# Kernel tuning notes

Measured on AMD Instinct MI355X. Metric: run time of the kernel, lower is better.

## Reference

```python
import jax, jax.numpy as jnp
import numpy as np

HIDDEN = 512
HEADS = 8
HEAD_DIM = HIDDEN // HEADS


def setup_inputs() -> dict:
    key = jax.random.key(0)
    ks = jax.random.split(key, 12)
    B, N, C = 4, 2048, HIDDEN
    s = 1.0 / np.sqrt(C)
    inp = {
        "query_content": jax.random.normal(ks[0], (B, N, C), dtype=jnp.float32),
        "query_pos": jax.random.uniform(ks[1], (B, N, 4), dtype=jnp.float32),
        "Wq": jax.random.uniform(ks[2], (C, C), jnp.float32, -s, s),
        "bq": jax.random.uniform(ks[3], (C,), jnp.float32, -s, s),
        "Wk": jax.random.uniform(ks[4], (C, C), jnp.float32, -s, s),
        "bk": jax.random.uniform(ks[5], (C,), jnp.float32, -s, s),
        "Wv": jax.random.uniform(ks[6], (C, C), jnp.float32, -s, s),
        "bv": jax.random.uniform(ks[7], (C,), jnp.float32, -s, s),
        "Wo": jax.random.uniform(ks[8], (C, C), jnp.float32, -s, s),
        "bo": jax.random.uniform(ks[9], (C,), jnp.float32, -s, s),
        "gamma": jnp.ones((C,), jnp.float32),
        "beta": jnp.zeros((C,), jnp.float32),
    }
    return inp


def _iof_bias(query_pos):
    # query_pos: [B, N, 4] -> bias [B, N, N] = -0.1 * sqrt(dx^2 + dy^2 + eps)
    x = query_pos[..., 0]
    y = query_pos[..., 1]
    dx = jnp.abs(x[:, :, None] - x[:, None, :])
    dy = jnp.abs(y[:, :, None] - y[:, None, :])
    dist = jnp.sqrt(dx * dx + dy * dy + 1e-8)
    return -0.1 * dist


def reference(query_content, query_pos, Wq, bq, Wk, bk, Wv, bv, Wo, bo, gamma, beta):
    B, N, C = query_content.shape
    H, D = HEADS, HEAD_DIM
    # torch Linear: x @ W.T + b
    Q = (query_content @ Wq.T + bq).reshape(B, N, H, D).transpose(0, 2, 1, 3)
    K = (query_content @ Wk.T + bk).reshape(B, N, H, D).transpose(0, 2, 1, 3)
    V = (query_content @ Wv.T + bv).reshape(B, N, H, D).transpose(0, 2, 1, 3)
    scores = jnp.einsum("bhnd,bhmd->bhnm", Q, K) / jnp.sqrt(jnp.float32(D))
    scores = scores + _iof_bias(query_pos)[:, None, :, :]
    attn = jax.nn.softmax(scores, axis=-1)
    out = jnp.einsum("bhnm,bhmd->bhnd", attn, V)
    out = out.transpose(0, 2, 1, 3).reshape(B, N, C)
    out = out @ Wo.T + bo
    h = out + query_content
    mu = jnp.mean(h, axis=-1, keepdims=True)
    var = jnp.var(h, axis=-1, keepdims=True)
    return (h - mu) / jnp.sqrt(var + 1e-5) * gamma + beta
```

## Files before the change

### kernel.cpp

```cpp
#include <hip/hip_runtime.h>
#include <hip/hip_bf16.h>

#define C_DIM 512
#define H_NUM 8
#define D_DIM 64
#define B_NUM 4
#define N_SEQ 2048
#define M_TOT (B_NUM*N_SEQ)

typedef unsigned short u16;
typedef unsigned int   u32;
typedef __attribute__((ext_vector_type(8))) short short8;
typedef __attribute__((ext_vector_type(4))) float f32x4;

#define MFMA16 __builtin_amdgcn_mfma_f32_16x16x32_bf16

__device__ __forceinline__ u16 f2b(float f) {
    union { float f; u32 u; } v; v.f = f;
    u32 r = v.u + 0x7FFFu + ((v.u >> 16) & 1u);
    return (u16)(r >> 16);
}
__device__ __forceinline__ float fexp2(float x) {
    float r;
    asm("v_exp_f32 %0, %1" : "=v"(r) : "v"(x));
    return r;
}
__device__ __forceinline__ float b2f_lo(u32 u) {
    union { u32 u; float f; } v; v.u = u << 16; return v.f;
}
__device__ __forceinline__ float b2f_hi(u32 u) {
    union { u32 u; float f; } v; v.u = u & 0xFFFF0000u; return v.f;
}
__device__ __forceinline__ void gload16(const u16* g, u16* l) {
    __builtin_amdgcn_global_load_lds(
        (const __attribute__((address_space(1))) void*)g,
        (__attribute__((address_space(3))) void*)l, 16, 0, 0);
}
__device__ __forceinline__ void cast8(const float* s, u16* d) {
    const float4* p = (const float4*)s;
    float4 a = p[0], b = p[1];
    short8 v;
    v[0] = (short)f2b(a.x); v[1] = (short)f2b(a.y);
    v[2] = (short)f2b(a.z); v[3] = (short)f2b(a.w);
    v[4] = (short)f2b(b.x); v[5] = (short)f2b(b.y);
    v[6] = (short)f2b(b.z); v[7] = (short)f2b(b.w);
    *(short8*)d = v;
}

__global__ __launch_bounds__(256) void k_prep(const float* __restrict__ qc,
                                              const float* __restrict__ Wq,
                                              const float* __restrict__ Wk,
                                              const float* __restrict__ Wv,
                                              const float* __restrict__ Wo,
                                              const float* __restrict__ bq,
                                              const float* __restrict__ bk,
                                              const float* __restrict__ bv,
                                              const float* __restrict__ bo,
                                              const float* __restrict__ qpos,
                                              u16* __restrict__ xb,
                                              u16* __restrict__ wb,
                                              float* __restrict__ bqkv,
                                              u16* __restrict__ bias)
{
    const int bid = blockIdx.x, t = threadIdx.x;
    if (bid < 2048) {
        int i = bid * 256 + t;
        cast8(qc + (size_t)i * 8, xb + (size_t)i * 8);
    } else if (bid < 2560) {
        int r = bid - 2048;
        int y = r >> 7;
        const float* s = (y == 0) ? Wq : (y == 1) ? Wk : (y == 2) ? Wv : Wo;
        int i = (r & 127) * 256 + t;
        cast8(s + (size_t)i * 8, wb + (size_t)y * 262144 + (size_t)i * 8);
    } else if (bid < 2568) {
        int idx = (bid - 2560) * 256 + t;
        float v = idx < 512 ? bq[idx] : idx < 1024 ? bk[idx - 512]
                : idx < 1536 ? bv[idx - 1024] : bo[idx - 1536];
        bqkv[idx] = v;
    } else {
        int r = bid - 2568;
        int i = r & 2047, b = r >> 11;
        const float4 qi = *(const float4*)(qpos + (size_t)(b * 2048 + i) * 4);
        const float4* pj = (const float4*)(qpos + ((size_t)b * 2048 + t * 8) * 4);
        const float NC = -0.1f * 1.4426950408889634f;
        short8 v;
        #pragma unroll
        for (int jj = 0; jj < 8; ++jj) {
            float4 pk = pj[jj];
            float dx = qi.x - pk.x, dy = qi.y - pk.y;
            float d2 = fmaf(dx, dx, fmaf(dy, dy, 1e-8f));
            v[jj] = (short)f2b(sqrtf(d2) * NC);
        }
        *(short8*)(bias + (size_t)(b * 2048 + i) * 2048 + t * 8) = v;
    }
}

__global__ __launch_bounds__(256) void k_gemm(const u16* __restrict__ A,
                                              const u16* __restrict__ Bw,
                                              const float* __restrict__ bias,
                                              const float* __restrict__ qc,
                                              u16* __restrict__ oq,
                                              u16* __restrict__ ok,
                                              u16* __restrict__ ov,
                                              float* __restrict__ outf,
                                              int fixed_mode)
{
    __shared__ alignas(16) u16 smem[24576];
    typedef u16 (*Tbuf)[4][128][8];
    Tbuf la = (Tbuf)smem;
    Tbuf lb = (Tbuf)(smem + 12288);
    const int t = threadIdx.x;
    const int nwg = gridDim.x * gridDim.y;
    const int wgid = blockIdx.y * gridDim.x + blockIdx.x;
    const int swz = (wgid & 7) * (nwg >> 3) + (wgid >> 3);
    const int ntn = gridDim.y;
    const int m0 = (swz / ntn) * 128, n0 = (swz % ntn) * 128;
    const int w = t >> 6, l = t & 63, lr = l & 15, kg = l >> 4;
    const int wm = w >> 1, wn = w & 1;
    const int NS = C_DIM / 32;

    f32x4 acc[4][4] = {};

    const int srow = t & 127;
    const u16* As0 = A + (size_t)(m0 + srow) * C_DIM + (t >> 7) * 8;
    const u16* Bs0 = Bw + (size_t)(n0 + srow) * C_DIM + (t >> 7) * 8;

    #pragma unroll
    for (int s = 0; s < 2; ++s) {
        u16* ldA = (u16*)la[s] + w * 512;
        u16* ldB = (u16*)lb[s] + w * 512;
        gload16(As0 + s * 32,      ldA);
        gload16(As0 + s * 32 + 16, ldA + 2048);
        gload16(Bs0 + s * 32,      ldB);
        gload16(Bs0 + s * 32 + 16, ldB + 2048);
    }
    asm volatile("s_waitcnt vmcnt(4)" ::: "memory");
    __builtin_amdgcn_s_barrier();

    for (int s = 0; s < NS; ++s) {
        const int bi = s % 3;
        if (s + 2 < NS) {
            const int bn = (s + 2) % 3;
            u16* ldA = (u16*)la[bn] + w * 512;
            u16* ldB = (u16*)lb[bn] + w * 512;
            gload16(As0 + (s + 2) * 32,      ldA);
            gload16(As0 + (s + 2) * 32 + 16, ldA + 2048);
            gload16(Bs0 + (s + 2) * 32,      ldB);
            gload16(Bs0 + (s + 2) * 32 + 16, ldB + 2048);
        }
        __builtin_amdgcn_sched_barrier(0);

        short8 af[4], bf[4];
        #pragma unroll
        for (int fm = 0; fm < 4; ++fm)
            af[fm] = *(const short8*)la[bi][kg][wm * 64 + fm * 16 + lr];
        #pragma unroll
        for (int fn = 0; fn < 4; ++fn)
            bf[fn] = *(const short8*)lb[bi][kg][wn * 64 + fn * 16 + lr];
        __builtin_amdgcn_s_setprio(1);
        #pragma unroll
        for (int fm = 0; fm < 4; ++fm)
        #pragma unroll
        for (int fn = 0; fn < 4; ++fn)
            acc[fm][fn] = MFMA16(af[fm], bf[fn], acc[fm][fn], 0, 0, 0);
        __builtin_amdgcn_s_setprio(0);

        if (s + 1 < NS) {
            if (s + 2 < NS) asm volatile("s_waitcnt vmcnt(4)" ::: "memory");
            else            asm volatile("s_waitcnt vmcnt(0)" ::: "memory");
            __builtin_amdgcn_s_barrier();
        }
    }

    const int mode = (fixed_mode == 3) ? 3 : (n0 >> 9);

    if (mode == 3) {
        #pragma unroll
        for (int fm = 0; fm < 4; ++fm)
        #pragma unroll
        for (int fn = 0; fn < 4; ++fn) {
            int c = n0 + wn * 64 + fn * 16 + lr;
            float bv_ = bias[c];
            #pragma unroll
            for (int i = 0; i < 4; ++i) {
                int m = m0 + wm * 64 + fm * 16 + kg * 4 + i;
                outf[(size_t)m * C_DIM + c] = acc[fm][fn][i] + bv_ + qc[(size_t)m * C_DIM + c];
            }
        }
        return;
    }

    __syncthreads();
    u16 (*tb)[132] = (u16(*)[132])smem;

    if (mode == 2) {
        #pragma unroll
        for (int fm = 0; fm < 4; ++fm)
        #pragma unroll
        for (int fn = 0; fn < 4; ++fn) {
            int c_loc = wn * 64 + fn * 16 + lr;
            float bv_ = bias[n0 + c_loc];
            #pragma unroll
            for (int i = 0; i < 4; ++i) {
                int m_loc = wm * 64 + fm * 16 + kg * 4 + i;
                tb[c_loc][m_loc] = f2b(acc[fm][fn][i] + bv_);
            }
        }
        __syncthreads();
        const int bb = m0 >> 11, nb = m0 & 2047;
        #pragma unroll
        for (int p = 0; p < 8; ++p) {
            int id = p * 256 + t;
            int row = id >> 4, seg = id & 15;
            short8 v = *(const short8*)&tb[row][seg * 8];
            int cc = (n0 & 511) + row;
            int h = cc >> 6, d = cc & 63;
            *(short8*)(ov + ((size_t)(bb * H_NUM + h) * D_DIM + d) * N_SEQ
                       + nb + seg * 8) = v;
        }
    } else {
        u16* outb = (mode == 0) ? oq : ok;
        #pragma unroll
        for (int fm = 0; fm < 4; ++fm)
        #pragma unroll
        for (int fn = 0; fn < 4; ++fn) {
            int c_loc = wn * 64 + fn * 16 + lr;
            float bv_ = bias[n0 + c_loc];
            #pragma unroll
            for (int i = 0; i < 4; ++i) {
                int m_loc = wm * 64 + fm * 16 + kg * 4 + i;
                tb[m_loc][c_loc] = f2b(acc[fm][fn][i] + bv_);
            }
        }
        __syncthreads();
        const int bb = m0 >> 11;
        #pragma unroll
        for (int p = 0; p < 8; ++p) {
            int id = p * 256 + t;
            int row = id >> 4, seg = id & 15;
            short8 v = *(const short8*)&tb[row][seg * 8];
            int m = m0 + row, n = m & 2047;
            int cc = (n0 & 511) + seg * 8;
            int h = cc >> 6, d = cc & 63;
            *(short8*)(outb + ((size_t)(bb * H_NUM + h) * N_SEQ + n) * D_DIM + d) = v;
        }
    }
}

__global__ __launch_bounds__(512, 4) void k_flash(const u16* __restrict__ Q,
                                                  const u16* __restrict__ K,
                                                  const u16* __restrict__ Vt,
                                                  const u16* __restrict__ bias,
                                                  u16* __restrict__ attn_out)
{
    __shared__ alignas(16) u16 kbuf[3][64][64];
    __shared__ alignas(16) u16 vbuf[3][64][64];
    __shared__ alignas(16) u16 pbuf[8][16][64];

    const int t = threadIdx.x;
    const int w = t >> 6, l = t & 63, lr = l & 15, g = l >> 4;
    const int flat = blockIdx.y * 16 + blockIdx.x;
    const int h = flat >> 6, b = (flat >> 4) & 3, qt = flat & 15;
    const int bh = b * H_NUM + h;
    const int q = qt * 128 + w * 16 + lr;
    const int sx = lr & 7;

    const float SC = 0.125f * 1.4426950408889634f;
    const int NT = N_SEQ / 64;

    const u16* Qb = Q + ((size_t)bh * N_SEQ + q) * D_DIM;
    const u16* Kb = K + (size_t)bh * N_SEQ * D_DIM;
    const u16* Vb = Vt + (size_t)bh * D_DIM * N_SEQ;
    const u16* Bb = bias + ((size_t)b * N_SEQ + q) * N_SEQ;

    short8 aq0 = *(const short8*)(Qb + g * 8);
    short8 aq1 = *(const short8*)(Qb + 32 + g * 8);

    const int sr = t >> 3;
    const int ssl = (t & 7) ^ (sr & 7);
    const u16* gK = Kb + (size_t)sr * D_DIM + ssl * 8;
    const u16* gV = Vb + (size_t)sr * N_SEQ + ssl * 8;

    f32x4 acc[4] = {};
    float lac0 = 0.f, lac1 = 0.f, lac2 = 0.f, lac3 = 0.f;
    uint2 bcur[4], bnxt[4];

    gload16(gK,              (u16*)&kbuf[0][0][0] + w * 512);
    gload16(gV,              (u16*)&vbuf[0][0][0] + w * 512);
    gload16(gK + 64 * D_DIM, (u16*)&kbuf[1][0][0] + w * 512);
    gload16(gV + 64,         (u16*)&vbuf[1][0][0] + w * 512);
    __builtin_amdgcn_sched_barrier(0);
    #pragma unroll
    for (int fn = 0; fn < 4; ++fn)
        bcur[fn] = *(const uint2*)(Bb + fn * 16 + g * 4);
    __builtin_amdgcn_sched_barrier(0);
    asm volatile("s_waitcnt vmcnt(6)" ::: "memory");
    __builtin_amdgcn_s_barrier();

    for (int kt = 0; kt < NT; ++kt) {
        const int bi = kt % 3;
        if (kt + 1 < NT) {
            #pragma unroll
            for (int fn = 0; fn < 4; ++fn)
                bnxt[fn] = *(const uint2*)(Bb + (kt + 1) * 64 + fn * 16 + g * 4);
        }
        __builtin_amdgcn_sched_barrier(0);
        if (kt + 2 < NT) {
            const int bn = (kt + 2) % 3;
            gload16(gK + (size_t)(kt + 2) * 64 * D_DIM, (u16*)&kbuf[bn][0][0] + w * 512);
            gload16(gV + (kt + 2) * 64,                 (u16*)&vbuf[bn][0][0] + w * 512);
        }
        __builtin_amdgcn_sched_barrier(0);

        f32x4 st[4] = {};
        __builtin_amdgcn_s_setprio(1);
        #pragma unroll
        for (int fn = 0; fn < 4; ++fn) {
            short8 ak0 = *(const short8*)&kbuf[bi][fn * 16 + lr][(g ^ sx) * 8];
            short8 ak1 = *(const short8*)&kbuf[bi][fn * 16 + lr][((4 + g) ^ sx) * 8];
            st[fn] = MFMA16(ak0, aq0, st[fn], 0, 0, 0);
            st[fn] = MFMA16(ak1, aq1, st[fn], 0, 0, 0);
        }
        __builtin_amdgcn_s_setprio(0);

        float sv[16];
        #pragma unroll
        for (int fn = 0; fn < 4; ++fn) {
            sv[fn * 4 + 0] = fmaf(st[fn][0], SC, b2f_lo(bcur[fn].x));
            sv[fn * 4 + 1] = fmaf(st[fn][1], SC, b2f_hi(bcur[fn].x));
            sv[fn * 4 + 2] = fmaf(st[fn][2], SC, b2f_lo(bcur[fn].y));
            sv[fn * 4 + 3] = fmaf(st[fn][3], SC, b2f_hi(bcur[fn].y));
        }
        #pragma unroll
        for (int j = 0; j < 4; ++j)  { sv[j]  = fexp2(sv[j]);  lac0 += sv[j]; }
        #pragma unroll
        for (int j = 4; j < 8; ++j)  { sv[j]  = fexp2(sv[j]);  lac1 += sv[j]; }
        #pragma unroll
        for (int j = 8; j < 12; ++j) { sv[j]  = fexp2(sv[j]);  lac2 += sv[j]; }
        #pragma unroll
        for (int j = 12; j < 16; ++j){ sv[j]  = fexp2(sv[j]);  lac3 += sv[j]; }

        #pragma unroll
        for (int fn = 0; fn < 4; ++fn) {
            union { float f; u32 u; } p0, p1, p2, p3;
            p0.f = sv[fn * 4 + 0]; p1.f = sv[fn * 4 + 1];
            p2.f = sv[fn * 4 + 2]; p3.f = sv[fn * 4 + 3];
            uint2 pk;
            pk.x = (p1.u & 0xFFFF0000u) | (p0.u >> 16);
            pk.y = (p3.u & 0xFFFF0000u) | (p2.u >> 16);
            int slot = fn * 2 + (g >> 1);
            *(uint2*)&pbuf[w][lr][(slot ^ sx) * 8 + (g & 1) * 4] = pk;
        }
        asm volatile("s_waitcnt lgkmcnt(0)" ::: "memory");
        __builtin_amdgcn_sched_barrier(0);

        short8 bp0 = *(const short8*)&pbuf[w][lr][(g ^ sx) * 8];
        short8 bp1 = *(const short8*)&pbuf[w][lr][((4 + g) ^ sx) * 8];

        __builtin_amdgcn_s_setprio(1);
        #pragma unroll
        for (int df = 0; df < 4; ++df) {
            short8 av0 = *(const short8*)&vbuf[bi][df * 16 + lr][(g ^ sx) * 8];
            short8 av1 = *(const short8*)&vbuf[bi][df * 16 + lr][((4 + g) ^ sx) * 8];
            acc[df] = MFMA16(av0, bp0, acc[df], 0, 0, 0);
            acc[df] = MFMA16(av1, bp1, acc[df], 0, 0, 0);
        }
        __builtin_amdgcn_s_setprio(0);

        #pragma unroll
        for (int fn = 0; fn < 4; ++fn) bcur[fn] = bnxt[fn];

        if (kt + 1 < NT) {
            if (kt + 2 < NT) asm volatile("s_waitcnt vmcnt(6)" ::: "memory");
            else             asm volatile("s_waitcnt vmcnt(4)" ::: "memory");
            __builtin_amdgcn_s_barrier();
        }
    }

    float l_run = (lac0 + lac1) + (lac2 + lac3);
    l_run += __shfl_xor(l_run, 16);
    l_run += __shfl_xor(l_run, 32);
    float rl;
    asm("v_rcp_f32 %0, %1" : "=v"(rl) : "v"(l_run));
    rl = rl * (2.f - l_run * rl);
    u16* ob = attn_out + ((size_t)(b * N_SEQ + q)) * C_DIM + h * D_DIM + g * 4;
    #pragma unroll
    for (int df = 0; df < 4; ++df) {
        u32 w0 = ((u32)f2b(acc[df][1] * rl) << 16) | f2b(acc[df][0] * rl);
        u32 w1 = ((u32)f2b(acc[df][3] * rl) << 16) | f2b(acc[df][2] * rl);
        uint2 pk; pk.x = w0; pk.y = w1;
        *(uint2*)(ob + df * 16) = pk;
    }
}

__global__ __launch_bounds__(256) void k_ln(const float* __restrict__ hbuf,
                                            const float* __restrict__ gamma,
                                            const float* __restrict__ beta,
                                            float* __restrict__ out)
{
    const int r = blockIdx.x;
    const int t = threadIdx.x;
    const size_t base = (size_t)r * C_DIM;
    float2 h01 = *(const float2*)(hbuf + base + t * 2);
    float s = h01.x + h01.y, sq = h01.x * h01.x + h01.y * h01.y;
    #pragma unroll
    for (int m = 1; m < 64; m <<= 1) {
        s += __shfl_xor(s, m);
        sq += __shfl_xor(sq, m);
    }
    __shared__ float ss[4], ssq[4];
    int w = t >> 6;
    if ((t & 63) == 0) { ss[w] = s; ssq[w] = sq; }
    __syncthreads();
    s = ss[0] + ss[1] + ss[2] + ss[3];
    sq = ssq[0] + ssq[1] + ssq[2] + ssq[3];
    float mu = s * (1.f / C_DIM);
    float var = sq * (1.f / C_DIM) - mu * mu;
    float inv = rsqrtf(var + 1e-5f);
    float2 g01 = *(const float2*)(gamma + t * 2);
    float2 b01 = *(const float2*)(beta + t * 2);
    float2 o;
    o.x = (h01.x - mu) * inv * g01.x + b01.x;
    o.y = (h01.y - mu) * inv * g01.y + b01.y;
    *(float2*)(out + base + t * 2) = o;
}

extern "C" void kernel_launch(void* const* d_in, const int* in_sizes, int n_in,
                              void* d_out, int out_size, void* d_ws, size_t ws_size,
                              hipStream_t stream)
{
    const float* qc    = (const float*)d_in[0];
    const float* qpos  = (const float*)d_in[1];
    const float* Wq    = (const float*)d_in[2];
    const float* bq    = (const float*)d_in[3];
    const float* Wk    = (const float*)d_in[4];
    const float* bk    = (const float*)d_in[5];
    const float* Wv    = (const float*)d_in[6];
    const float* bv    = (const float*)d_in[7];
    const float* Wo    = (const float*)d_in[8];
    const float* bo    = (const float*)d_in[9];
    const float* gamma = (const float*)d_in[10];
    const float* beta  = (const float*)d_in[11];
    float* out = (float*)d_out;

    char* ws = (char*)d_ws;
    const size_t MB = 1024 * 1024;
    u16*   bias_ws = (u16*)(ws);
    u16*   xb_ws   = (u16*)(ws + 32 * MB);
    u16*   wb_ws   = (u16*)(ws + 40 * MB);
    float* bqkv_ws = (float*)(ws + 42 * MB);
    u16*   q_ws    = (u16*)(ws + 43 * MB);
    u16*   k_ws    = (u16*)(ws + 51 * MB);
    u16*   v_ws    = (u16*)(ws + 59 * MB);
    u16*   a_ws    = (u16*)(ws + 75 * MB);
    float* p_ws    = (float*)(ws + 43 * MB);

    k_prep<<<dim3(10760), 256, 0, stream>>>(qc, Wq, Wk, Wv, Wo, bq, bk, bv, bo,
                                            qpos, xb_ws, wb_ws, bqkv_ws, bias_ws);
    k_gemm<<<dim3(M_TOT / 128, 12), 256, 0, stream>>>(xb_ws, wb_ws, bqkv_ws, nullptr,
                                                      q_ws, k_ws, v_ws, nullptr, -1);
    k_flash<<<dim3(16, 32), 512, 0, stream>>>(q_ws, k_ws, v_ws, bias_ws, a_ws);
    k_gemm<<<dim3(M_TOT / 128, 4), 256, 0, stream>>>(a_ws, wb_ws + 1536 * 512,
                                                     bqkv_ws + 1536, qc,
                                                     nullptr, nullptr, nullptr, p_ws, 3);
    k_ln<<<dim3(M_TOT), 256, 0, stream>>>(p_ws, gamma, beta, out);
}
```

Before: 163.3 us.

## Enlarge GEMM tiles to 256x128 and overlap bias-matrix build with QKV GEMM

```diff
diff --git a/kernel.cpp b/kernel.cpp
--- a/kernel.cpp
+++ b/kernel.cpp
@@ -56,11 +56,9 @@
                                               const float* __restrict__ bk,
                                               const float* __restrict__ bv,
                                               const float* __restrict__ bo,
-                                              const float* __restrict__ qpos,
                                               u16* __restrict__ xb,
                                               u16* __restrict__ wb,
-                                              float* __restrict__ bqkv,
-                                              u16* __restrict__ bias)
+                                              float* __restrict__ bqkv)
 {
     const int bid = blockIdx.x, t = threadIdx.x;
     if (bid < 2048) {
@@ -72,16 +70,35 @@
         const float* s = (y == 0) ? Wq : (y == 1) ? Wk : (y == 2) ? Wv : Wo;
         int i = (r & 127) * 256 + t;
         cast8(s + (size_t)i * 8, wb + (size_t)y * 262144 + (size_t)i * 8);
-    } else if (bid < 2568) {
+    } else {
         int idx = (bid - 2560) * 256 + t;
         float v = idx < 512 ? bq[idx] : idx < 1024 ? bk[idx - 512]
                 : idx < 1536 ? bv[idx - 1024] : bo[idx - 1536];
         bqkv[idx] = v;
-    } else {
-        int r = bid - 2568;
-        int i = r & 2047, b = r >> 11;
+    }
+}
+
+__global__ __launch_bounds__(512, 2) void k_gemm(const u16* __restrict__ A,
+                                                 const u16* __restrict__ Bw,
+                                                 const float* __restrict__ bias,
+                                                 const float* __restrict__ qc,
+                                                 u16* __restrict__ oq,
+                                                 u16* __restrict__ ok,
+                                                 u16* __restrict__ ov,
+                                                 float* __restrict__ outf,
+                                                 int fixed_mode,
+                                                 const float* __restrict__ qpos,
+                                                 u16* __restrict__ biasm)
+{
+    __shared__ alignas(16) u16 smem[36864];
+    const int bid = blockIdx.x, t = threadIdx.x;
+
+    if (fixed_mode == -1 && bid >= 384) {
+        int ig = (bid - 384) * 2 + (t >> 8);
+        int i = ig & 2047, b = ig >> 11;
+        int j8 = t & 255;
         const float4 qi = *(const float4*)(qpos + (size_t)(b * 2048 + i) * 4);
-        const float4* pj = (const float4*)(qpos + ((size_t)b * 2048 + t * 8) * 4);
+        const float4* pj = (const float4*)(qpos + ((size_t)b * 2048 + j8 * 8) * 4);
         const float NC = -0.1f * 1.4426950408889634f;
         short8 v;
         #pragma unroll
@@ -91,72 +108,56 @@
             float d2 = fmaf(dx, dx, fmaf(dy, dy, 1e-8f));
             v[jj] = (short)f2b(sqrtf(d2) * NC);
         }
-        *(short8*)(bias + (size_t)(b * 2048 + i) * 2048 + t * 8) = v;
-    }
-}
-
-__global__ __launch_bounds__(256) void k_gemm(const u16* __restrict__ A,
-                                              const u16* __restrict__ Bw,
-                                              const float* __restrict__ bias,
-                                              const float* __restrict__ qc,
-                                              u16* __restrict__ oq,
-                                              u16* __restrict__ ok,
-                                              u16* __restrict__ ov,
-                                              float* __restrict__ outf,
-                                              int fixed_mode)
-{
-    __shared__ alignas(16) u16 smem[24576];
-    typedef u16 (*Tbuf)[4][128][8];
-    Tbuf la = (Tbuf)smem;
-    Tbuf lb = (Tbuf)(smem + 12288);
-    const int t = threadIdx.x;
-    const int nwg = gridDim.x * gridDim.y;
-    const int wgid = blockIdx.y * gridDim.x + blockIdx.x;
-    const int swz = (wgid & 7) * (nwg >> 3) + (wgid >> 3);
-    const int ntn = gridDim.y;
-    const int m0 = (swz / ntn) * 128, n0 = (swz % ntn) * 128;
+        *(short8*)(biasm + (size_t)(b * 2048 + i) * 2048 + j8 * 8) = v;
+        return;
+    }
+
+    u16* laB = smem;
+    u16* lbB = smem + 24576;
+    const int nwg = (fixed_mode == 3) ? 128 : 384;
+    const int ntn = (fixed_mode == 3) ? 4 : 12;
+    const int swz = (bid & 7) * (nwg >> 3) + (bid >> 3);
+    const int m0 = (swz / ntn) * 256, n0 = (swz % ntn) * 128;
     const int w = t >> 6, l = t & 63, lr = l & 15, kg = l >> 4;
     const int wm = w >> 1, wn = w & 1;
     const int NS = C_DIM / 32;
 
     f32x4 acc[4][4] = {};
 
-    const int srow = t & 127;
-    const u16* As0 = A + (size_t)(m0 + srow) * C_DIM + (t >> 7) * 8;
-    const u16* Bs0 = Bw + (size_t)(n0 + srow) * C_DIM + (t >> 7) * 8;
-
-    #pragma unroll
-    for (int s = 0; s < 2; ++s) {
-        u16* ldA = (u16*)la[s] + w * 512;
-        u16* ldB = (u16*)lb[s] + w * 512;
-        gload16(As0 + s * 32,      ldA);
-        gload16(As0 + s * 32 + 16, ldA + 2048);
-        gload16(Bs0 + s * 32,      ldB);
-        gload16(Bs0 + s * 32 + 16, ldB + 2048);
-    }
-    asm volatile("s_waitcnt vmcnt(4)" ::: "memory");
+    const int arow = t & 255, akoct = t >> 8;
+    const int brow = t & 127, bkoct = t >> 7;
+    const u16* As0 = A + (size_t)(m0 + arow) * C_DIM + akoct * 8;
+    const u16* Bs0 = Bw + (size_t)(n0 + brow) * C_DIM + bkoct * 8;
+
+#define GSTAGE(buf, k0) { \
+    u16* ldA = laB + (buf) * 8192; \
+    u16* ldB = lbB + (buf) * 4096; \
+    gload16(As0 + (k0),      ldA + w * 512); \
+    gload16(As0 + (k0) + 16, ldA + 4096 + w * 512); \
+    gload16(Bs0 + (k0),      ldB + w * 512); }
+
+    GSTAGE(0, 0)
+    GSTAGE(1, 32)
+    asm volatile("s_waitcnt vmcnt(3)" ::: "memory");
     __builtin_amdgcn_s_barrier();
 
     for (int s = 0; s < NS; ++s) {
         const int bi = s % 3;
         if (s + 2 < NS) {
             const int bn = (s + 2) % 3;
-            u16* ldA = (u16*)la[bn] + w * 512;
-            u16* ldB = (u16*)lb[bn] + w * 512;
-            gload16(As0 + (s + 2) * 32,      ldA);
-            gload16(As0 + (s + 2) * 32 + 16, ldA + 2048);
-            gload16(Bs0 + (s + 2) * 32,      ldB);
-            gload16(Bs0 + (s + 2) * 32 + 16, ldB + 2048);
+            GSTAGE(bn, (s + 2) * 32)
         }
         __builtin_amdgcn_sched_barrier(0);
 
+        const u16* laS = laB + bi * 8192 + kg * 2048;
+        const u16* lbS = lbB + bi * 4096 + kg * 1024;
         short8 af[4], bf[4];
         #pragma unroll
         for (int fm = 0; fm < 4; ++fm)
-            af[fm] = *(const short8*)la[bi][kg][wm * 64 + fm * 16 + lr];
+            af[fm] = *(const short8*)(laS + (wm * 64 + fm * 16 + lr) * 8);
         #pragma unroll
         for (int fn = 0; fn < 4; ++fn)
-            bf[fn] = *(const short8*)lb[bi][kg][wn * 64 + fn * 16 + lr];
+            bf[fn] = *(const short8*)(lbS + (wn * 64 + fn * 16 + lr) * 8);
         __builtin_amdgcn_s_setprio(1);
         #pragma unroll
         for (int fm = 0; fm < 4; ++fm)
@@ -166,11 +167,12 @@
         __builtin_amdgcn_s_setprio(0);
 
         if (s + 1 < NS) {
-            if (s + 2 < NS) asm volatile("s_waitcnt vmcnt(4)" ::: "memory");
+            if (s + 2 < NS) asm volatile("s_waitcnt vmcnt(3)" ::: "memory");
             else            asm volatile("s_waitcnt vmcnt(0)" ::: "memory");
             __builtin_amdgcn_s_barrier();
         }
     }
+#undef GSTAGE
 
     const int mode = (fixed_mode == 3) ? 3 : (n0 >> 9);
 
@@ -191,9 +193,9 @@
     }
 
     __syncthreads();
-    u16 (*tb)[132] = (u16(*)[132])smem;
 
     if (mode == 2) {
+        u16 (*tb)[260] = (u16(*)[260])smem;
         #pragma unroll
         for (int fm = 0; fm < 4; ++fm)
         #pragma unroll
@@ -210,8 +212,8 @@
         const int bb = m0 >> 11, nb = m0 & 2047;
         #pragma unroll
         for (int p = 0; p < 8; ++p) {
-            int id = p * 256 + t;
-            int row = id >> 4, seg = id & 15;
+            int id = p * 512 + t;
+            int row = id >> 5, seg = id & 31;
             short8 v = *(const short8*)&tb[row][seg * 8];
             int cc = (n0 & 511) + row;
             int h = cc >> 6, d = cc & 63;
@@ -220,6 +222,7 @@
         }
     } else {
         u16* outb = (mode == 0) ? oq : ok;
+        u16 (*tb)[132] = (u16(*)[132])smem;
         #pragma unroll
         for (int fm = 0; fm < 4; ++fm)
         #pragma unroll
@@ -236,7 +239,7 @@
         const int bb = m0 >> 11;
         #pragma unroll
         for (int p = 0; p < 8; ++p) {
-            int id = p * 256 + t;
+            int id = p * 512 + t;
             int row = id >> 4, seg = id & 15;
             short8 v = *(const short8*)&tb[row][seg * 8];
             int m = m0 + row, n = m & 2047;
@@ -455,13 +458,15 @@
     u16*   a_ws    = (u16*)(ws + 75 * MB);
     float* p_ws    = (float*)(ws + 43 * MB);
 
-    k_prep<<<dim3(10760), 256, 0, stream>>>(qc, Wq, Wk, Wv, Wo, bq, bk, bv, bo,
-                                            qpos, xb_ws, wb_ws, bqkv_ws, bias_ws);
-    k_gemm<<<dim3(M_TOT / 128, 12), 256, 0, stream>>>(xb_ws, wb_ws, bqkv_ws, nullptr,
-                                                      q_ws, k_ws, v_ws, nullptr, -1);
+    k_prep<<<dim3(2568), 256, 0, stream>>>(qc, Wq, Wk, Wv, Wo, bq, bk, bv, bo,
+                                           xb_ws, wb_ws, bqkv_ws);
+    k_gemm<<<dim3(4480), 512, 0, stream>>>(xb_ws, wb_ws, bqkv_ws, nullptr,
+                                           q_ws, k_ws, v_ws, nullptr, -1,
+                                           qpos, bias_ws);
     k_flash<<<dim3(16, 32), 512, 0, stream>>>(q_ws, k_ws, v_ws, bias_ws, a_ws);
-    k_gemm<<<dim3(M_TOT / 128, 4), 256, 0, stream>>>(a_ws, wb_ws + 1536 * 512,
-                                                     bqkv_ws + 1536, qc,
-                                                     nullptr, nullptr, nullptr, p_ws, 3);
+    k_gemm<<<dim3(128), 512, 0, stream>>>(a_ws, wb_ws + 1536 * 512,
+                                          bqkv_ws + 1536, qc,
+                                          nullptr, nullptr, nullptr, p_ws, 3,
+                                          nullptr, nullptr);
     k_ln<<<dim3(M_TOT), 256, 0, stream>>>(p_ws, gamma, beta, out);
 }
```

New measurement: 170.3 us. +4.3%, slower.
